# Kernel optimization log

Hardware: AMD Instinct MI355X
Metric: run time of the kernel (lower is better)

Reference implementation:

```python
import jax, jax.numpy as jnp
import numpy as np


def setup_inputs() -> dict:
    key = jax.random.key(0)
    k1, k2, k3 = jax.random.split(key, 3)
    # N, C, H, W per input_specs
    x = jax.random.normal(k1, (16, 8, 1024, 1024), dtype=jnp.float32)
    # weight: (out_channels, in_channels, kH, kW)
    weight = jax.random.normal(k2, (8, 8, 3, 3), dtype=jnp.float32) * 0.1
    bias = jax.random.normal(k3, (8,), dtype=jnp.float32) * 0.1
    return {"x": x, "weight": weight, "bias": bias}


def reference(x, weight, bias):
    # DietConv2dV2's tiled per-kernel-column matmul loop is mathematically a
    # standard direct conv2d (stride=1, padding=1) followed by a bias add.
    out = jax.lax.conv_general_dilated(
        x, weight,
        window_strides=(1, 1),
        padding=((1, 1), (1, 1)),
        dimension_numbers=("NCHW", "OIHW", "NCHW"),
    )
    return out + bias[None, :, None, None]
```

## Files before the change

kernel.cpp:

```cpp
#include <hip/hip_runtime.h>
#include <hip/hip_bf16.h>


typedef __attribute__((ext_vector_type(8))) short short8;
typedef __attribute__((ext_vector_type(4))) float f32x4;

#define HH 1024
#define WW 1024
#define HWsz (1024*1024)
#define WB 64
#define HB 8
#define SROWS 10
#define UROW 72
#define NIT 32
#define NSITES (SROWS*UROW)

__device__ __forceinline__ int pk2(float a, float b) {
    __hip_bfloat162 h = __float22bfloat162_rn(make_float2(a, b));
    return *reinterpret_cast<int*>(&h);
}
__device__ __forceinline__ unsigned short f2bf(float f) {
    unsigned u = __float_as_uint(f);
    return (unsigned short)((u + 0x7FFFu + ((u >> 16) & 1u)) >> 16);
}

__global__ __launch_bounds__(256) void conv3x3_reg(
    const float* __restrict__ x,
    const float* __restrict__ wgt,
    const float* __restrict__ bias,
    float* __restrict__ out)
{
    __shared__ int4 bfA[NSITES];
    __shared__ int4 bfB[NSITES];

    const int tid  = threadIdx.x;
    const int lane = tid & 63;
    const int wv   = tid >> 6;
    const int l15  = lane & 15;
    const int ch   = lane >> 4;

    const int wx    = blockIdx.x;
    const int strip = blockIdx.y;
    const int n     = blockIdx.z;
    const int w0    = wx * WB;
    const int htbase = strip * (NIT * HB);

    const float* xn = x + (size_t)n * 8 * HWsz;
    const float* base0 = xn + 0 * (size_t)HWsz;
    const float* base1 = xn + 1 * (size_t)HWsz;
    const float* base2 = xn + 2 * (size_t)HWsz;
    const float* base3 = xn + 3 * (size_t)HWsz;
    const float* base4 = xn + 4 * (size_t)HWsz;
    const float* base5 = xn + 5 * (size_t)HWsz;
    const float* base6 = xn + 6 * (size_t)HWsz;
    const float* base7 = xn + 7 * (size_t)HWsz;

    const int t0  = ch;
    const int kh0 = (t0 >= 3) ? 1 : 0;
    const int kw0 = t0 - 3 * kh0;
    const int t1  = 4 + ch;
    const int kh1 = (t1 >= 6) ? 2 : 1;
    const int kw1 = t1 - 3 * kh1;
    const int off0 = kh0 * UROW + kw0 + 3;
    const int off1 = kh1 * UROW + kw1 + 3;
    const int off2 = 2 * UROW + 2 + 3;

    const int  coc = (l15 < 8) ? l15 : 7;
    const bool com = (l15 < 8);
    short8 b0, b1, b2;
    {
        const float* wp0 = wgt + coc * 72 + kh0 * 3 + kw0;
        const float* wp1 = wgt + coc * 72 + kh1 * 3 + kw1;
        const float* wp2 = wgt + coc * 72 + 2 * 3 + 2;
#pragma unroll
        for (int j = 0; j < 8; ++j) {
            b0[j] = (short)(com ? f2bf(wp0[j * 9]) : 0);
            b1[j] = (short)(com ? f2bf(wp1[j * 9]) : 0);
            b2[j] = (short)((com && ch == 0) ? f2bf(wp2[j * 9]) : 0);
        }
    }
    const float bv = com ? bias[l15] : 0.0f;

    int srow[3], gwc[3];
    bool wok[3], sv[3];
#pragma unroll
    for (int j = 0; j < 3; ++j) {
        const int s = tid + j * 256;
        sv[j]   = (s < NSITES);
        const int r = s / UROW;
        const int u = s - r * UROW;
        srow[j] = r;
        const int gwr = w0 - 4 + u;
        wok[j]  = ((unsigned)gwr < (unsigned)WW);
        gwc[j]  = (gwr < 0) ? 0 : ((gwr > WW - 1) ? WW - 1 : gwr);
    }

    float bkA[3][8], bkB[3][8];

#define LOADS(htile, bk)                                                     \
    {                                                                        \
        _Pragma("unroll")                                                    \
        for (int j = 0; j < 3; ++j) {                                        \
            const int gr  = (htile) - 1 + srow[j];                           \
            const int ghc = (gr < 0) ? 0 : ((gr > HH - 1) ? HH - 1 : gr);    \
            const unsigned voff = ((unsigned)(ghc * WW + gwc[j])) * 4u;      \
            asm volatile("global_load_dword %0, %8, %9\n\t"                  \
                         "global_load_dword %1, %8, %10\n\t"                 \
                         "global_load_dword %2, %8, %11\n\t"                 \
                         "global_load_dword %3, %8, %12\n\t"                 \
                         "global_load_dword %4, %8, %13\n\t"                 \
                         "global_load_dword %5, %8, %14\n\t"                 \
                         "global_load_dword %6, %8, %15\n\t"                 \
                         "global_load_dword %7, %8, %16"                     \
                         : "=v"(bk[j][0]), "=v"(bk[j][1]), "=v"(bk[j][2]),   \
                           "=v"(bk[j][3]), "=v"(bk[j][4]), "=v"(bk[j][5]),   \
                           "=v"(bk[j][6]), "=v"(bk[j][7])                    \
                         : "v"(voff), "s"(base0), "s"(base1), "s"(base2),    \
                           "s"(base3), "s"(base4), "s"(base5), "s"(base6),   \
                           "s"(base7)                                        \
                         : "memory");                                        \
        }                                                                    \
    }

#define CONV(htile, bk, bfb)                                                 \
    {                                                                        \
        _Pragma("unroll")                                                    \
        for (int j = 0; j < 3; ++j) {                                        \
            if (sv[j]) {                                                     \
                const int gr = (htile) - 1 + srow[j];                        \
                const bool ok = ((unsigned)gr < (unsigned)HH) && wok[j];     \
                const float v0 = ok ? bk[j][0] : 0.0f;                       \
                const float v1 = ok ? bk[j][1] : 0.0f;                       \
                const float v2 = ok ? bk[j][2] : 0.0f;                       \
                const float v3 = ok ? bk[j][3] : 0.0f;                       \
                const float v4 = ok ? bk[j][4] : 0.0f;                       \
                const float v5 = ok ? bk[j][5] : 0.0f;                       \
                const float v6 = ok ? bk[j][6] : 0.0f;                       \
                const float v7 = ok ? bk[j][7] : 0.0f;                       \
                int4 pk;                                                     \
                pk.x = pk2(v0, v1);                                          \
                pk.y = pk2(v2, v3);                                          \
                pk.z = pk2(v4, v5);                                          \
                pk.w = pk2(v6, v7);                                          \
                (bfb)[tid + j * 256] = pk;                                   \
            }                                                                \
        }                                                                    \
    }

#define BODY(htile, bsrc)                                                    \
    {                                                                        \
        f32x4 acc[2][4];                                                     \
        _Pragma("unroll")                                                    \
        for (int th = 0; th < 2; ++th)                                       \
            _Pragma("unroll")                                                \
            for (int wt = 0; wt < 4; ++wt) {                                 \
                acc[th][wt].x = bv; acc[th][wt].y = bv;                      \
                acc[th][wt].z = bv; acc[th][wt].w = bv;                      \
            }                                                                \
        _Pragma("unroll")                                                    \
        for (int th = 0; th < 2; ++th) {                                     \
            const int hl = wv * 2 + th;                                      \
            const int ub = hl * UROW + l15;                                  \
            _Pragma("unroll")                                                \
            for (int wt = 0; wt < 4; ++wt) {                                 \
                const int u = ub + wt * 16;                                  \
                short8 a0 = *reinterpret_cast<const short8*>(&(bsrc)[u + off0]); \
                short8 a1 = *reinterpret_cast<const short8*>(&(bsrc)[u + off1]); \
                short8 a2 = *reinterpret_cast<const short8*>(&(bsrc)[u + off2]); \
                f32x4 c = acc[th][wt];                                       \
                c = __builtin_amdgcn_mfma_f32_16x16x32_bf16(a0, b0, c, 0, 0, 0); \
                c = __builtin_amdgcn_mfma_f32_16x16x32_bf16(a1, b1, c, 0, 0, 0); \
                c = __builtin_amdgcn_mfma_f32_16x16x32_bf16(a2, b2, c, 0, 0, 0); \
                acc[th][wt] = c;                                             \
            }                                                                \
        }                                                                    \
        if (com) {                                                           \
            _Pragma("unroll")                                                \
            for (int th = 0; th < 2; ++th) {                                 \
                const int hl = wv * 2 + th;                                  \
                float* op = out + ((size_t)n * 8 + l15) * HWsz               \
                                + (size_t)((htile) + hl) * WW + w0 + ch * 4; \
                _Pragma("unroll")                                            \
                for (int wt = 0; wt < 4; ++wt)                               \
                    *reinterpret_cast<float4*>(op + wt * 16) =               \
                        *reinterpret_cast<const float4*>(&acc[th][wt]);      \
            }                                                                \
        }                                                                    \
    }

    LOADS(htbase, bkA);

    for (int k = 0; k < NIT; k += 2) {
        {
            const int ht  = htbase + k * HB;
            LOADS(ht + HB, bkB);
            if (k == 0) {
                asm volatile("s_waitcnt vmcnt(24)" ::: "memory");
            } else {
                asm volatile("s_waitcnt vmcnt(32)" ::: "memory");
            }
            __builtin_amdgcn_sched_barrier(0);
            CONV(ht, bkA, bfA);
            asm volatile("s_waitcnt lgkmcnt(0)" ::: "memory");
            __builtin_amdgcn_sched_barrier(0);
            __builtin_amdgcn_s_barrier();
            BODY(ht, bfA);
        }
        {
            const int ht  = htbase + (k + 1) * HB;
            int t2 = k + 2; if (t2 > NIT - 1) t2 = NIT - 1;
            LOADS(htbase + t2 * HB, bkA);
            asm volatile("s_waitcnt vmcnt(32)" ::: "memory");
            __builtin_amdgcn_sched_barrier(0);
            CONV(ht, bkB, bfB);
            asm volatile("s_waitcnt lgkmcnt(0)" ::: "memory");
            __builtin_amdgcn_sched_barrier(0);
            __builtin_amdgcn_s_barrier();
            BODY(ht, bfB);
        }
    }
#undef LOADS
#undef CONV
#undef BODY
}

extern "C" void kernel_launch(void* const* d_in, const int* in_sizes, int n_in,
                              void* d_out, int out_size, void* d_ws, size_t ws_size,
                              hipStream_t stream) {
    const float* x    = (const float*)d_in[0];
    const float* wgt  = (const float*)d_in[1];
    const float* bias = (const float*)d_in[2];
    float* out = (float*)d_out;

    dim3 grid(16, 4, 16);
    dim3 block(256, 1, 1);
    conv3x3_reg<<<grid, block, 0, stream>>>(x, wgt, bias, out);
}
```

Before: 276.6 us.

## Pack two output rows per MFMA N-dimension to fill idle output-channel lanes

Result: no change. 275.3 us (-0.5%).

```diff
diff --git a/kernel.cpp b/kernel.cpp
--- a/kernel.cpp
+++ b/kernel.cpp
@@ -12,7 +12,7 @@
 #define HB 8
 #define SROWS 10
 #define UROW 72
-#define NIT 32
+#define NIT 16
 #define NSITES (SROWS*UROW)
 
 __device__ __forceinline__ int pk2(float a, float b) {
@@ -24,7 +24,7 @@
     return (unsigned short)((u + 0x7FFFu + ((u >> 16) & 1u)) >> 16);
 }
 
-__global__ __launch_bounds__(256) void conv3x3_reg(
+__global__ __launch_bounds__(256) void conv3x3_pack2(
     const float* __restrict__ x,
     const float* __restrict__ wgt,
     const float* __restrict__ bias,
@@ -55,31 +55,29 @@
     const float* base6 = xn + 6 * (size_t)HWsz;
     const float* base7 = xn + 7 * (size_t)HWsz;
 
-    const int t0  = ch;
-    const int kh0 = (t0 >= 3) ? 1 : 0;
-    const int kw0 = t0 - 3 * kh0;
-    const int t1  = 4 + ch;
-    const int kh1 = (t1 >= 6) ? 2 : 1;
-    const int kw1 = t1 - 3 * kh1;
+    const int s0 = 8 * ch,      kh0 = s0 / 24, kw0 = (s0 % 24) / 8;
+    const int s1 = 32 + 8 * ch, kh1 = s1 / 24, kw1 = (s1 % 24) / 8;
+    const int s2 = 64 + 8 * ch, kh2 = s2 / 24, kw2 = (s2 % 24) / 8;
     const int off0 = kh0 * UROW + kw0 + 3;
     const int off1 = kh1 * UROW + kw1 + 3;
-    const int off2 = 2 * UROW + 2 + 3;
-
-    const int  coc = (l15 < 8) ? l15 : 7;
-    const bool com = (l15 < 8);
+    const int off2 = kh2 * UROW + kw2 + 3;
+
+    const int hi  = l15 >> 3;
+    const int co8 = l15 & 7;
     short8 b0, b1, b2;
     {
-        const float* wp0 = wgt + coc * 72 + kh0 * 3 + kw0;
-        const float* wp1 = wgt + coc * 72 + kh1 * 3 + kw1;
-        const float* wp2 = wgt + coc * 72 + 2 * 3 + 2;
+        const int ke0 = kh0 - hi, ke1 = kh1 - hi, ke2 = kh2 - hi;
+        const bool v0 = (ke0 >= 0) && (ke0 <= 2);
+        const bool v1 = (ke1 >= 0) && (ke1 <= 2);
+        const bool v2 = (ke2 >= 0) && (ke2 <= 2);
 #pragma unroll
         for (int j = 0; j < 8; ++j) {
-            b0[j] = (short)(com ? f2bf(wp0[j * 9]) : 0);
-            b1[j] = (short)(com ? f2bf(wp1[j * 9]) : 0);
-            b2[j] = (short)((com && ch == 0) ? f2bf(wp2[j * 9]) : 0);
+            b0[j] = (short)(v0 ? f2bf(wgt[co8 * 72 + j * 9 + ke0 * 3 + kw0]) : 0);
+            b1[j] = (short)(v1 ? f2bf(wgt[co8 * 72 + j * 9 + ke1 * 3 + kw1]) : 0);
+            b2[j] = (short)(v2 ? f2bf(wgt[co8 * 72 + j * 9 + ke2 * 3 + kw2]) : 0);
         }
     }
-    const float bv = com ? bias[l15] : 0.0f;
+    const float bv = bias[co8];
 
     int srow[3], gwc[3];
     bool wok[3], sv[3];
@@ -149,55 +147,42 @@
 
 #define BODY(htile, bsrc)                                                    \
     {                                                                        \
-        f32x4 acc[2][4];                                                     \
-        _Pragma("unroll")                                                    \
-        for (int th = 0; th < 2; ++th)                                       \
-            _Pragma("unroll")                                                \
-            for (int wt = 0; wt < 4; ++wt) {                                 \
-                acc[th][wt].x = bv; acc[th][wt].y = bv;                      \
-                acc[th][wt].z = bv; acc[th][wt].w = bv;                      \
-            }                                                                \
-        _Pragma("unroll")                                                    \
-        for (int th = 0; th < 2; ++th) {                                     \
-            const int hl = wv * 2 + th;                                      \
-            const int ub = hl * UROW + l15;                                  \
-            _Pragma("unroll")                                                \
-            for (int wt = 0; wt < 4; ++wt) {                                 \
-                const int u = ub + wt * 16;                                  \
-                short8 a0 = *reinterpret_cast<const short8*>(&(bsrc)[u + off0]); \
-                short8 a1 = *reinterpret_cast<const short8*>(&(bsrc)[u + off1]); \
-                short8 a2 = *reinterpret_cast<const short8*>(&(bsrc)[u + off2]); \
-                f32x4 c = acc[th][wt];                                       \
-                c = __builtin_amdgcn_mfma_f32_16x16x32_bf16(a0, b0, c, 0, 0, 0); \
-                c = __builtin_amdgcn_mfma_f32_16x16x32_bf16(a1, b1, c, 0, 0, 0); \
-                c = __builtin_amdgcn_mfma_f32_16x16x32_bf16(a2, b2, c, 0, 0, 0); \
-                acc[th][wt] = c;                                             \
-            }                                                                \
-        }                                                                    \
-        if (com) {                                                           \
-            _Pragma("unroll")                                                \
-            for (int th = 0; th < 2; ++th) {                                 \
-                const int hl = wv * 2 + th;                                  \
-                float* op = out + ((size_t)n * 8 + l15) * HWsz               \
-                                + (size_t)((htile) + hl) * WW + w0 + ch * 4; \
-                _Pragma("unroll")                                            \
-                for (int wt = 0; wt < 4; ++wt)                               \
-                    *reinterpret_cast<float4*>(op + wt * 16) =               \
-                        *reinterpret_cast<const float4*>(&acc[th][wt]);      \
-            }                                                                \
-        }                                                                    \
+        f32x4 acc[4];                                                        \
+        _Pragma("unroll")                                                    \
+        for (int wt = 0; wt < 4; ++wt) {                                     \
+            acc[wt].x = bv; acc[wt].y = bv; acc[wt].z = bv; acc[wt].w = bv;  \
+        }                                                                    \
+        const int ub = (2 * wv) * UROW + l15;                                \
+        _Pragma("unroll")                                                    \
+        for (int wt = 0; wt < 4; ++wt) {                                     \
+            const int u = ub + wt * 16;                                      \
+            short8 a0 = *reinterpret_cast<const short8*>(&(bsrc)[u + off0]); \
+            short8 a1 = *reinterpret_cast<const short8*>(&(bsrc)[u + off1]); \
+            short8 a2 = *reinterpret_cast<const short8*>(&(bsrc)[u + off2]); \
+            f32x4 c = acc[wt];                                               \
+            c = __builtin_amdgcn_mfma_f32_16x16x32_bf16(a0, b0, c, 0, 0, 0); \
+            c = __builtin_amdgcn_mfma_f32_16x16x32_bf16(a1, b1, c, 0, 0, 0); \
+            c = __builtin_amdgcn_mfma_f32_16x16x32_bf16(a2, b2, c, 0, 0, 0); \
+            acc[wt] = c;                                                     \
+        }                                                                    \
+        float* op = out + ((size_t)n * 8 + co8) * HWsz                       \
+                        + (size_t)((htile) + 2 * wv + hi) * WW + w0 + ch * 4;\
+        _Pragma("unroll")                                                    \
+        for (int wt = 0; wt < 4; ++wt)                                       \
+            *reinterpret_cast<float4*>(op + wt * 16) =                       \
+                *reinterpret_cast<const float4*>(&acc[wt]);                  \
     }
 
     LOADS(htbase, bkA);
 
     for (int k = 0; k < NIT; k += 2) {
         {
-            const int ht  = htbase + k * HB;
+            const int ht = htbase + k * HB;
             LOADS(ht + HB, bkB);
             if (k == 0) {
                 asm volatile("s_waitcnt vmcnt(24)" ::: "memory");
             } else {
-                asm volatile("s_waitcnt vmcnt(32)" ::: "memory");
+                asm volatile("s_waitcnt vmcnt(28)" ::: "memory");
             }
             __builtin_amdgcn_sched_barrier(0);
             CONV(ht, bkA, bfA);
@@ -207,10 +192,10 @@
             BODY(ht, bfA);
         }
         {
-            const int ht  = htbase + (k + 1) * HB;
+            const int ht = htbase + (k + 1) * HB;
             int t2 = k + 2; if (t2 > NIT - 1) t2 = NIT - 1;
             LOADS(htbase + t2 * HB, bkA);
-            asm volatile("s_waitcnt vmcnt(32)" ::: "memory");
+            asm volatile("s_waitcnt vmcnt(28)" ::: "memory");
             __builtin_amdgcn_sched_barrier(0);
             CONV(ht, bkB, bfB);
             asm volatile("s_waitcnt lgkmcnt(0)" ::: "memory");
@@ -232,7 +217,7 @@
     const float* bias = (const float*)d_in[2];
     float* out = (float*)d_out;
 
-    dim3 grid(16, 4, 16);
+    dim3 grid(16, 8, 16);
     dim3 block(256, 1, 1);
-    conv3x3_reg<<<grid, block, 0, stream>>>(x, wgt, bias, out);
-}
+    conv3x3_pack2<<<grid, block, 0, stream>>>(x, wgt, bias, out);
+}
```
